# Kernel tuning notes

Measured on AMD Instinct MI355X. Metric: run time of the kernel, lower is better.

Reference implementation:

```python
import jax, jax.numpy as jnp
import numpy as np

B, N, L, E = 4, 8, 2048, 16384
CH = [128, 256, 256, 256]
EPS = 1e-5
USE_MAX = True


def setup_inputs() -> dict:
    key = jax.random.key(0)
    ks = jax.random.split(key, 10)
    d = {}
    d["x"] = jax.random.normal(ks[0], (B, N, CH[0], L), jnp.float32)
    d["edge_index"] = jax.random.randint(ks[1], (2, E), 0, L, dtype=jnp.int32)
    wspecs = [("W1", CH[0], CH[1]), ("W2", CH[1], CH[2]), ("W3", CH[2], CH[3]),
              ("W1s", CH[0], CH[1]), ("W2s", CH[1], CH[2]), ("W3s", CH[2], CH[3])]
    for i, (nm, ci, co) in enumerate(wspecs):
        std = (2.0 / (ci + co)) ** 0.5  # xavier_normal
        d[nm] = std * jax.random.normal(ks[2 + i], (ci, co), jnp.float32)
        d["b" + nm[1:]] = jnp.zeros((co,), jnp.float32)
    for nm, co in [("1", CH[1]), ("2", CH[2]), ("3", CH[3]),
                   ("1s", CH[1]), ("2s", CH[2]), ("3s", CH[3])]:
        d["g" + nm] = jnp.ones((co,), jnp.float32)
        d["be" + nm] = jnp.zeros((co,), jnp.float32)
    return d


def _gcn_norm(edge_index, num_nodes):
    # PyG gcn_norm with improved=True: A_hat = A + 2I, sym normalization.
    src, dst = edge_index[0], edge_index[1]
    loop = jnp.arange(num_nodes, dtype=src.dtype)
    src = jnp.concatenate([src, loop])
    dst = jnp.concatenate([dst, loop])
    w = jnp.concatenate([jnp.ones((edge_index.shape[1],), jnp.float32),
                         jnp.full((num_nodes,), 2.0, jnp.float32)])
    deg = jnp.zeros((num_nodes,), jnp.float32).at[dst].add(w)
    dis = jnp.where(deg > 0, jax.lax.rsqrt(deg), 0.0)
    return src, dst, dis[src] * w * dis[dst]


def _gcn(h, W, bias, src, dst, norm, num_nodes):
    # h: [G, L, Cin] node features for G independent copies of the shared graph
    hw = h @ W  # [G, L, Cout]
    msgs = hw[:, src, :] * norm[None, :, None]  # gather along nodes
    agg = jnp.zeros((h.shape[0], num_nodes, W.shape[1]), h.dtype).at[:, dst].add(msgs)
    return agg + bias


def _bn(x, g, be):
    # x: [Nb, C, L]; training-mode BatchNorm1d over (Nb, L) per channel
    m = x.mean(axis=(0, 2), keepdims=True)
    v = x.var(axis=(0, 2), keepdims=True)
    return g[None, :, None] * (x - m) * jax.lax.rsqrt(v + EPS) + be[None, :, None]


def _forward(x, edge_index, params):
    b, n, c, l = x.shape
    src, dst, norm = _gcn_norm(edge_index, l)
    xo = None
    for (W, bias, Ws, bs, g, be, gs, bes) in params:
        # per-element branch
        h = x.reshape(b * n, x.shape[2], l).transpose(0, 2, 1)  # [b*n, L, C]
        x1 = _gcn(h, W, bias, src, dst, norm, l).transpose(0, 2, 1)  # [b*n, Cout, L]
        x1 = _bn(x1, g, be)
        # symmetric pooled branch
        xp = jnp.max(x, axis=1) if USE_MAX else jnp.sum(x, axis=1)  # [b, C, L]
        x2 = _gcn(xp.transpose(0, 2, 1), Ws, bs, src, dst, norm, l).transpose(0, 2, 1)
        x2 = _bn(x2, gs, bes)
        co = x2.shape[1]
        x2 = jnp.broadcast_to(x2[:, None], (b, n, co, l)).reshape(b * n, co, l)
        xo = jax.nn.relu(x1 + x2)  # [b*n, Cout, L]
        x = xo.reshape(b, n, co, l)
    return xo  # final output is [b*n, CH[3], L] (not reshaped back)


def reference(x, edge_index, W1, b1, W2, b2, W3, b3, W1s, b1s, W2s, b2s, W3s, b3s,
              g1, be1, g2, be2, g3, be3, g1s, be1s, g2s, be2s, g3s, be3s):
    params = [(W1, b1, W1s, b1s, g1, be1, g1s, be1s),
              (W2, b2, W2s, b2s, g2, be2, g2s, be2s),
              (W3, b3, W3s, b3s, g3, be3, g3s, be3s)]
    return _forward(x, edge_index, params)
```

## Files before the change

kernel.cpp:

```cpp
#include <hip/hip_runtime.h>
#include <math.h>

#define LNODES 2048
#define NEDGE 16384
#define GBIG 32
#define GSM 4
#define NCOUT 256
#define BN_EPS 1e-5f
#define ND 32

typedef unsigned short u16;
typedef __attribute__((ext_vector_type(8))) short bf16x8;
typedef __attribute__((ext_vector_type(4))) float f32x4;

__device__ __forceinline__ unsigned pk2(float a, float b) {
  unsigned ua = __float_as_uint(a); ua += 0x7fffu + ((ua >> 16) & 1u);
  unsigned ub = __float_as_uint(b); ub += 0x7fffu + ((ub >> 16) & 1u);
  return (ua >> 16) | (ub & 0xffff0000u);
}
__device__ __forceinline__ float blo(unsigned u) { return __uint_as_float(u << 16); }
__device__ __forceinline__ float bhi(unsigned u) { return __uint_as_float(u & 0xffff0000u); }

__device__ __forceinline__ void gl16(const u16* g, u16* l) {
  __builtin_amdgcn_global_load_lds(
      (const __attribute__((address_space(1))) void*)g,
      (__attribute__((address_space(3))) void*)l, 16, 0, 0);
}


__global__ __launch_bounds__(256) void count_deg_k(const int* __restrict__ ei,
                                                   float* __restrict__ deg,
                                                   int* __restrict__ cnt) {
  int e = blockIdx.x * 256 + threadIdx.x;
  if (e < NEDGE) {
    int d = ei[NEDGE + e];
    atomicAdd(&deg[d], 1.0f);
    atomicAdd(&cnt[d], 1);
  }
}

__global__ __launch_bounds__(256) void dis_k(const float* __restrict__ deg,
                                             float* __restrict__ dis,
                                             float* __restrict__ selfn) {
  int i = blockIdx.x * 256 + threadIdx.x;
  if (i < LNODES) {
    float di = rsqrtf(deg[i] + 2.0f);
    dis[i] = di;
    selfn[i] = 2.0f * di * di;
  }
}

__global__ __launch_bounds__(256) void scan_k(const int* __restrict__ cnt,
                                              int* __restrict__ rp) {
  __shared__ int part[256];
  int t = threadIdx.x;
  int base = t * 8;
  int loc[8];
  int s = 0;
#pragma unroll
  for (int j = 0; j < 8; ++j) { loc[j] = s; s += cnt[base + j]; }
  part[t] = s;
  __syncthreads();
  for (int off = 1; off < 256; off <<= 1) {
    int v = (t >= off) ? part[t - off] : 0;
    __syncthreads();
    part[t] += v;
    __syncthreads();
  }
  int excl = (t == 0) ? 0 : part[t - 1];
#pragma unroll
  for (int j = 0; j < 8; ++j) rp[base + j] = excl + loc[j];
  if (t == 255) rp[LNODES] = part[255];
}

__global__ __launch_bounds__(256) void fill_k(const int* __restrict__ ei,
                                              const int* __restrict__ rp,
                                              int* __restrict__ fillc,
                                              const float* __restrict__ dis,
                                              int* __restrict__ col,
                                              float* __restrict__ wn) {
  int e = blockIdx.x * 256 + threadIdx.x;
  if (e < NEDGE) {
    int s = ei[e], d = ei[NEDGE + e];
    int pos = rp[d] + atomicAdd(&fillc[d], 1);
    col[pos] = s;
    wn[pos] = dis[s] * dis[d];
  }
}

__global__ __launch_bounds__(256) void trans_k(const float* __restrict__ X,
                                               u16* __restrict__ XT, int Cin) {
  __shared__ float T[64][65];
  const int g = blockIdx.z;
  const int n0 = blockIdx.x * 64;
  const int c0 = blockIdx.y * 64;
  const int tr = threadIdx.x >> 4;
  const int tc = (threadIdx.x & 15) * 4;
#pragma unroll
  for (int p = 0; p < 4; ++p) {
    int ci = c0 + tr + p * 16;
    float4 v = *reinterpret_cast<const float4*>(&X[((size_t)g * Cin + ci) * LNODES + n0 + tc]);
    T[tr + p * 16][tc + 0] = v.x; T[tr + p * 16][tc + 1] = v.y;
    T[tr + p * 16][tc + 2] = v.z; T[tr + p * 16][tc + 3] = v.w;
  }
  __syncthreads();
#pragma unroll
  for (int p = 0; p < 4; ++p) {
    int nd = tr + p * 16;
    uint2 o = {pk2(T[tc + 0][nd], T[tc + 1][nd]), pk2(T[tc + 2][nd], T[tc + 3][nd])};
    *reinterpret_cast<uint2*>(&XT[((size_t)g * LNODES + n0 + nd) * Cin + c0 + tc]) = o;
  }
}

struct WCvt {
  const float* src[6];
  u16* dst[6];
  int ci[6];
};
__global__ __launch_bounds__(256) void cvtw_all_k(WCvt wp) {
  __shared__ float T[64][65];
  const int w = blockIdx.z;
  const int Ci = wp.ci[w];
  const int ci0 = blockIdx.y * 64;
  if (ci0 >= Ci) return;
  const float* W = wp.src[w];
  u16* WT = wp.dst[w];
  const int co0 = blockIdx.x * 64;
  const int tr = threadIdx.x >> 4;
  const int tc = (threadIdx.x & 15) * 4;
#pragma unroll
  for (int p = 0; p < 4; ++p) {
    int ci = ci0 + tr + p * 16;
    float4 v = *reinterpret_cast<const float4*>(&W[(size_t)ci * NCOUT + co0 + tc]);
    T[tr + p * 16][tc + 0] = v.x; T[tr + p * 16][tc + 1] = v.y;
    T[tr + p * 16][tc + 2] = v.z; T[tr + p * 16][tc + 3] = v.w;
  }
  __syncthreads();
#pragma unroll
  for (int p = 0; p < 4; ++p) {
    int co = tr + p * 16;
    uint2 o = {pk2(T[tc + 0][co], T[tc + 1][co]), pk2(T[tc + 2][co], T[tc + 3][co])};
    *reinterpret_cast<uint2*>(&WT[(size_t)(co0 + co) * Ci + ci0 + tc]) = o;
  }
}

__global__ __launch_bounds__(256) void pool_bf_k(const u16* __restrict__ X,
                                                 u16* __restrict__ XP, int per) {
  int i = blockIdx.x * 256 + threadIdx.x;
  size_t f = (size_t)i * 8;
  int b = (int)(f / per);
  size_t rem = f - (size_t)b * per;
  const u16* base = X + (size_t)b * 8 * per + rem;
  uint4 u = *reinterpret_cast<const uint4*>(base);
  float m0 = blo(u.x), m1 = bhi(u.x), m2 = blo(u.y), m3 = bhi(u.y);
  float m4 = blo(u.z), m5 = bhi(u.z), m6 = blo(u.w), m7 = bhi(u.w);
#pragma unroll
  for (int j = 1; j < 8; ++j) {
    uint4 v = *reinterpret_cast<const uint4*>(base + (size_t)j * per);
    m0 = fmaxf(m0, blo(v.x)); m1 = fmaxf(m1, bhi(v.x));
    m2 = fmaxf(m2, blo(v.y)); m3 = fmaxf(m3, bhi(v.y));
    m4 = fmaxf(m4, blo(v.z)); m5 = fmaxf(m5, bhi(v.z));
    m6 = fmaxf(m6, blo(v.w)); m7 = fmaxf(m7, bhi(v.w));
  }
  uint4 o = {pk2(m0, m1), pk2(m2, m3), pk2(m4, m5), pk2(m6, m7)};
  *reinterpret_cast<uint4*>(XP + (size_t)b * per + rem) = o;
}

__device__ __forceinline__ void coef_ld(const float* __restrict__ st,
                                        const float* __restrict__ ga,
                                        const float* __restrict__ be,
                                        const float* __restrict__ gs,
                                        const float* __restrict__ bes,
                                        float* lk1, float* lk2, float* lcc, int t) {
  float sA = 0.f, qA = 0.f, sB = 0.f, qB = 0.f;
#pragma unroll
  for (int x = 0; x < 8; ++x) {
    sA += st[x * NCOUT + t];
    qA += st[2048 + x * NCOUT + t];
    sB += st[4096 + x * NCOUT + t];
    qB += st[6144 + x * NCOUT + t];
  }
  const float c1 = (float)(GBIG * LNODES), c2 = (float)(GSM * LNODES);
  float mA = sA / c1;
  float vA = qA / c1 - mA * mA;
  float kA = ga[t] * rsqrtf(vA + BN_EPS);
  float mB = sB / c2;
  float vB = qB / c2 - mB * mB;
  float kB = gs[t] * rsqrtf(vB + BN_EPS);
  lk1[t] = kA;
  lk2[t] = kB;
  lcc[t] = be[t] - kA * mA + bes[t] - kB * mB;
}

template <int Cin>
__global__ __launch_bounds__(256) void gemm_k(const u16* __restrict__ Xbig,
                                              const u16* __restrict__ xp,
                                              const u16* __restrict__ WbT,
                                              const u16* __restrict__ WsT,
                                              u16* __restrict__ HW1,
                                              u16* __restrict__ hw2) {
  __shared__ u16 smem[17408];
  u16* Ash = smem;
  u16* Bsh = smem + 4096;
  const int z = blockIdx.z;
  const bool sym = z < GSM;
  const int g = sym ? z : z - GSM;
  const u16* Wmat = sym ? WsT : WbT;
  const u16* Xmat = sym ? xp : Xbig;
  u16* out = sym ? hw2 : HW1;
  const int n0 = blockIdx.x * 128;
  const int c0 = blockIdx.y * 128;
  const int t = threadIdx.x;
  const int wv = t >> 6;
  const int lane = t & 63;
  const int q = lane >> 4, l = lane & 15;
  const int wm = wv >> 1, wn = wv & 1;
  f32x4 zero = {0.f, 0.f, 0.f, 0.f};
  f32x4 acc[4][4];
#pragma unroll
  for (int i = 0; i < 4; ++i)
#pragma unroll
    for (int j = 0; j < 4; ++j) acc[i][j] = zero;
  const int r0 = t >> 2;
  const int seg = (t & 3) * 8;
  const u16* Wg = Wmat + (size_t)(c0 + r0) * Cin + seg;
  const u16* Xg = Xmat + ((size_t)g * LNODES + n0 + r0) * Cin + seg;
  const size_t rstep = (size_t)64 * Cin;
  for (int k0 = 0; k0 < Cin; k0 += 32) {
    if (k0) __syncthreads();
    gl16(Wg + k0, &Ash[t * 8]);
    gl16(Wg + rstep + k0, &Ash[2048 + t * 8]);
    gl16(Xg + k0, &Bsh[t * 8]);
    gl16(Xg + rstep + k0, &Bsh[2048 + t * 8]);
    __syncthreads();
    bf16x8 af[4], bx[4];
#pragma unroll
    for (int fi = 0; fi < 4; ++fi)
      af[fi] = *reinterpret_cast<const bf16x8*>(&Ash[(wm * 64 + fi * 16 + l) * 32 + q * 8]);
#pragma unroll
    for (int fj = 0; fj < 4; ++fj)
      bx[fj] = *reinterpret_cast<const bf16x8*>(&Bsh[(wn * 64 + fj * 16 + l) * 32 + q * 8]);
#pragma unroll
    for (int fi = 0; fi < 4; ++fi)
#pragma unroll
      for (int fj = 0; fj < 4; ++fj)
        acc[fi][fj] = __builtin_amdgcn_mfma_f32_16x16x32_bf16(af[fi], bx[fj], acc[fi][fj], 0, 0, 0);
  }
  __syncthreads();
  u16* Csh = smem;
#pragma unroll
  for (int fi = 0; fi < 4; ++fi) {
#pragma unroll
    for (int fj = 0; fj < 4; ++fj) {
      int co_l = wm * 64 + fi * 16 + q * 4;
      int nd_l = wn * 64 + fj * 16 + l;
      uint2 pkd = {pk2(acc[fi][fj][0], acc[fi][fj][1]),
                   pk2(acc[fi][fj][2], acc[fi][fj][3])};
      *reinterpret_cast<uint2*>(&Csh[nd_l * 136 + co_l]) = pkd;
    }
  }
  __syncthreads();
#pragma unroll
  for (int p = 0; p < 8; ++p) {
    int idx = p * 256 + t;
    int nd = idx >> 4;
    int c8 = (idx & 15) * 8;
    uint4 v = *reinterpret_cast<const uint4*>(&Csh[nd * 136 + c8]);
    *reinterpret_cast<uint4*>(&out[((size_t)g * LNODES + n0 + nd) * NCOUT + c0 + c8]) = v;
  }
}

__global__ __launch_bounds__(256) void agg_comb_k(const u16* __restrict__ HW1,
                                                  const u16* __restrict__ hw2,
                                                  const int* __restrict__ col,
                                                  const float* __restrict__ wn,
                                                  const int* __restrict__ rp,
                                                  const float* __restrict__ selfn,
                                                  u16* __restrict__ AGG1,
                                                  u16* __restrict__ agg2,
                                                  float* __restrict__ st) {
  __shared__ float lsum[8][NCOUT], lsq[8][NCOUT];
  const int bid = blockIdx.x;
  const int t = threadIdx.x;
  const int wv = t >> 6;
  float* sumO;
  float* sqO;
  int shard;
  if (bid < 1024) {
    int slot = bid >> 3;
    int chunk = slot & 63;
    int g0 = (bid & 7) + 8 * (slot >> 6);
    const int d0 = chunk * ND;
    const int h = (t >> 5) & 1;
    const int ch = (t & 31) * 8;
    const u16* baseh = HW1 + (size_t)(g0 + 16 * h) * LNODES * NCOUT;
    u16* outh = AGG1 + (size_t)(g0 + 16 * h) * LNODES * NCOUT;
    float s0 = 0.f, s1 = 0.f, s2 = 0.f, s3 = 0.f, s4 = 0.f, s5 = 0.f, s6 = 0.f, s7 = 0.f;
    float q0 = 0.f, q1 = 0.f, q2 = 0.f, q3 = 0.f, q4 = 0.f, q5 = 0.f, q6 = 0.f, q7 = 0.f;
    for (int i = wv; i < ND; i += 4) {
      int d = d0 + i;
      int e0 = rp[d], e1 = rp[d + 1];
      float sw = selfn[d];
      uint4 u = *reinterpret_cast<const uint4*>(&baseh[(size_t)d * NCOUT + ch]);
      float a0 = sw * blo(u.x), a1 = sw * bhi(u.x), a2 = sw * blo(u.y), a3 = sw * bhi(u.y);
      float a4 = sw * blo(u.z), a5 = sw * bhi(u.z), a6 = sw * blo(u.w), a7 = sw * bhi(u.w);
      int e = e0;
      const int e4 = e0 + ((e1 - e0) & ~3);
      for (; e < e4; e += 4) {
        int i0 = col[e + 0], i1 = col[e + 1], i2 = col[e + 2], i3 = col[e + 3];
        float w0 = wn[e + 0], w1 = wn[e + 1], w2 = wn[e + 2], w3 = wn[e + 3];
        uint4 v0 = *reinterpret_cast<const uint4*>(&baseh[(size_t)i0 * NCOUT + ch]);
        uint4 v1 = *reinterpret_cast<const uint4*>(&baseh[(size_t)i1 * NCOUT + ch]);
        uint4 v2 = *reinterpret_cast<const uint4*>(&baseh[(size_t)i2 * NCOUT + ch]);
        uint4 v3 = *reinterpret_cast<const uint4*>(&baseh[(size_t)i3 * NCOUT + ch]);
        a0 += w0 * blo(v0.x); a1 += w0 * bhi(v0.x); a2 += w0 * blo(v0.y); a3 += w0 * bhi(v0.y);
        a4 += w0 * blo(v0.z); a5 += w0 * bhi(v0.z); a6 += w0 * blo(v0.w); a7 += w0 * bhi(v0.w);
        a0 += w1 * blo(v1.x); a1 += w1 * bhi(v1.x); a2 += w1 * blo(v1.y); a3 += w1 * bhi(v1.y);
        a4 += w1 * blo(v1.z); a5 += w1 * bhi(v1.z); a6 += w1 * blo(v1.w); a7 += w1 * bhi(v1.w);
        a0 += w2 * blo(v2.x); a1 += w2 * bhi(v2.x); a2 += w2 * blo(v2.y); a3 += w2 * bhi(v2.y);
        a4 += w2 * blo(v2.z); a5 += w2 * bhi(v2.z); a6 += w2 * blo(v2.w); a7 += w2 * bhi(v2.w);
        a0 += w3 * blo(v3.x); a1 += w3 * bhi(v3.x); a2 += w3 * blo(v3.y); a3 += w3 * bhi(v3.y);
        a4 += w3 * blo(v3.z); a5 += w3 * bhi(v3.z); a6 += w3 * blo(v3.w); a7 += w3 * bhi(v3.w);
      }
      for (; e < e1; ++e) {
        int ci = col[e];
        float w = wn[e];
        uint4 v = *reinterpret_cast<const uint4*>(&baseh[(size_t)ci * NCOUT + ch]);
        a0 += w * blo(v.x); a1 += w * bhi(v.x); a2 += w * blo(v.y); a3 += w * bhi(v.y);
        a4 += w * blo(v.z); a5 += w * bhi(v.z); a6 += w * blo(v.w); a7 += w * bhi(v.w);
      }
      uint4 o = {pk2(a0, a1), pk2(a2, a3), pk2(a4, a5), pk2(a6, a7)};
      *reinterpret_cast<uint4*>(&outh[(size_t)d * NCOUT + ch]) = o;
      s0 += a0; s1 += a1; s2 += a2; s3 += a3; s4 += a4; s5 += a5; s6 += a6; s7 += a7;
      q0 += a0 * a0; q1 += a1 * a1; q2 += a2 * a2; q3 += a3 * a3;
      q4 += a4 * a4; q5 += a5 * a5; q6 += a6 * a6; q7 += a7 * a7;
    }
    int row = wv * 2 + h;
    float4 sa = {s0, s1, s2, s3}, sb = {s4, s5, s6, s7};
    float4 qa = {q0, q1, q2, q3}, qb = {q4, q5, q6, q7};
    *reinterpret_cast<float4*>(&lsum[row][ch]) = sa;
    *reinterpret_cast<float4*>(&lsum[row][ch + 4]) = sb;
    *reinterpret_cast<float4*>(&lsq[row][ch]) = qa;
    *reinterpret_cast<float4*>(&lsq[row][ch + 4]) = qb;
    sumO = st; sqO = st + 2048; shard = (bid & 7) * NCOUT;
  } else {
    int b2 = bid - 1024;
    int g = b2 & (GSM - 1);
    int chunk = b2 >> 2;
    const int d0 = chunk * ND;
    const int lc = (t & 63) * 4;
    const u16* base = hw2 + (size_t)g * LNODES * NCOUT;
    float4 s = {0.f, 0.f, 0.f, 0.f}, qq = {0.f, 0.f, 0.f, 0.f};
    for (int i = wv; i < ND; i += 4) {
      int d = d0 + i;
      int e0 = rp[d], e1 = rp[d + 1];
      float sw = selfn[d];
      uint2 u = *reinterpret_cast<const uint2*>(&base[(size_t)d * NCOUT + lc]);
      float4 a = {sw * blo(u.x), sw * bhi(u.x), sw * blo(u.y), sw * bhi(u.y)};
      int e = e0;
      const int e4 = e0 + ((e1 - e0) & ~3);
      for (; e < e4; e += 4) {
        int i0 = col[e + 0], i1 = col[e + 1], i2 = col[e + 2], i3 = col[e + 3];
        float w0 = wn[e + 0], w1 = wn[e + 1], w2 = wn[e + 2], w3 = wn[e + 3];
        uint2 v0 = *reinterpret_cast<const uint2*>(&base[(size_t)i0 * NCOUT + lc]);
        uint2 v1 = *reinterpret_cast<const uint2*>(&base[(size_t)i1 * NCOUT + lc]);
        uint2 v2 = *reinterpret_cast<const uint2*>(&base[(size_t)i2 * NCOUT + lc]);
        uint2 v3 = *reinterpret_cast<const uint2*>(&base[(size_t)i3 * NCOUT + lc]);
        a.x += w0 * blo(v0.x); a.y += w0 * bhi(v0.x); a.z += w0 * blo(v0.y); a.w += w0 * bhi(v0.y);
        a.x += w1 * blo(v1.x); a.y += w1 * bhi(v1.x); a.z += w1 * blo(v1.y); a.w += w1 * bhi(v1.y);
        a.x += w2 * blo(v2.x); a.y += w2 * bhi(v2.x); a.z += w2 * blo(v2.y); a.w += w2 * bhi(v2.y);
        a.x += w3 * blo(v3.x); a.y += w3 * bhi(v3.x); a.z += w3 * blo(v3.y); a.w += w3 * bhi(v3.y);
      }
      for (; e < e1; ++e) {
        float w = wn[e];
        uint2 v = *reinterpret_cast<const uint2*>(&base[(size_t)col[e] * NCOUT + lc]);
        a.x += w * blo(v.x); a.y += w * bhi(v.x); a.z += w * blo(v.y); a.w += w * bhi(v.y);
      }
      uint2 o = {pk2(a.x, a.y), pk2(a.z, a.w)};
      *reinterpret_cast<uint2*>(&agg2[((size_t)g * LNODES + d) * NCOUT + lc]) = o;
      s.x += a.x; s.y += a.y; s.z += a.z; s.w += a.w;
      qq.x += a.x * a.x; qq.y += a.y * a.y; qq.z += a.z * a.z; qq.w += a.w * a.w;
    }
    *reinterpret_cast<float4*>(&lsum[wv][lc]) = s;
    *reinterpret_cast<float4*>(&lsq[wv][lc]) = qq;
    float4 z4 = {0.f, 0.f, 0.f, 0.f};
    *reinterpret_cast<float4*>(&lsum[wv + 4][lc]) = z4;
    *reinterpret_cast<float4*>(&lsq[wv + 4][lc]) = z4;
    sumO = st + 4096; sqO = st + 6144; shard = (b2 & 7) * NCOUT;
  }
  __syncthreads();
  float ts = 0.f, tq = 0.f;
#pragma unroll
  for (int r = 0; r < 8; ++r) {
    ts += lsum[r][t];
    tq += lsq[r][t];
  }
  atomicAdd(&sumO[shard + t], ts);
  atomicAdd(&sqO[shard + t], tq);
}

__global__ __launch_bounds__(256) void fuse_k(const u16* __restrict__ A1,
                                              const u16* __restrict__ A2,
                                              const float* __restrict__ st,
                                              const float* __restrict__ ga,
                                              const float* __restrict__ be,
                                              const float* __restrict__ gs,
                                              const float* __restrict__ bes,
                                              u16* __restrict__ Xf,
                                              u16* __restrict__ xpo) {
  __shared__ __align__(16) float lk1[NCOUT];
  __shared__ __align__(16) float lk2[NCOUT];
  __shared__ __align__(16) float lcc[NCOUT];
  const int t = threadIdx.x;
  coef_ld(st, ga, be, gs, bes, lk1, lk2, lcc, t);
  __syncthreads();
  const int b = blockIdx.y;
  const int idx = blockIdx.x * 256 + t;
  const int node = idx >> 5;
  const int ch = (idx & 31) * 8;
  float K1[8], K2[8], CC[8];
#pragma unroll
  for (int j = 0; j < 8; ++j) {
    K1[j] = lk1[ch + j]; K2[j] = lk2[ch + j]; CC[j] = lcc[ch + j];
  }
  const size_t off2 = ((size_t)b * LNODES + node) * NCOUT + ch;
  uint4 a2 = *reinterpret_cast<const uint4*>(&A2[off2]);
  float t0 = K2[0] * blo(a2.x) + CC[0], t1 = K2[1] * bhi(a2.x) + CC[1];
  float t2 = K2[2] * blo(a2.y) + CC[2], t3 = K2[3] * bhi(a2.y) + CC[3];
  float t4 = K2[4] * blo(a2.z) + CC[4], t5 = K2[5] * bhi(a2.z) + CC[5];
  float t6 = K2[6] * blo(a2.w) + CC[6], t7 = K2[7] * bhi(a2.w) + CC[7];
  float m0 = 0.f, m1 = 0.f, m2 = 0.f, m3 = 0.f, m4 = 0.f, m5 = 0.f, m6 = 0.f, m7 = 0.f;
  const size_t step = (size_t)LNODES * NCOUT;
  const size_t base1 = ((size_t)(b * 8) * LNODES + node) * NCOUT + ch;
#pragma unroll
  for (int n = 0; n < 8; ++n) {
    uint4 a1 = *reinterpret_cast<const uint4*>(&A1[base1 + n * step]);
    float o0 = fmaxf(K1[0] * blo(a1.x) + t0, 0.f);
    float o1 = fmaxf(K1[1] * bhi(a1.x) + t1, 0.f);
    float o2 = fmaxf(K1[2] * blo(a1.y) + t2, 0.f);
    float o3 = fmaxf(K1[3] * bhi(a1.y) + t3, 0.f);
    float o4 = fmaxf(K1[4] * blo(a1.z) + t4, 0.f);
    float o5 = fmaxf(K1[5] * bhi(a1.z) + t5, 0.f);
    float o6 = fmaxf(K1[6] * blo(a1.w) + t6, 0.f);
    float o7 = fmaxf(K1[7] * bhi(a1.w) + t7, 0.f);
    uint4 ov = {pk2(o0, o1), pk2(o2, o3), pk2(o4, o5), pk2(o6, o7)};
    *reinterpret_cast<uint4*>(&Xf[base1 + n * step]) = ov;
    m0 = fmaxf(m0, o0); m1 = fmaxf(m1, o1); m2 = fmaxf(m2, o2); m3 = fmaxf(m3, o3);
    m4 = fmaxf(m4, o4); m5 = fmaxf(m5, o5); m6 = fmaxf(m6, o6); m7 = fmaxf(m7, o7);
  }
  uint4 mo = {pk2(m0, m1), pk2(m2, m3), pk2(m4, m5), pk2(m6, m7)};
  *reinterpret_cast<uint4*>(&xpo[off2]) = mo;
}

__global__ __launch_bounds__(256) void fuse_tr_bf_k(const u16* __restrict__ A1,
                                                    const u16* __restrict__ A2,
                                                    const float* __restrict__ st,
                                                    const float* __restrict__ ga,
                                                    const float* __restrict__ be,
                                                    const float* __restrict__ gs,
                                                    const float* __restrict__ bes,
                                                    float* __restrict__ O) {
  __shared__ float T[64][65];
  __shared__ float lk1[NCOUT], lk2[NCOUT], lcc[NCOUT];
  const int g = blockIdx.z;
  const int d0 = blockIdx.x * 64;
  const int c0 = blockIdx.y * 64;
  const int b = g >> 3;
  const int t = threadIdx.x;
  coef_ld(st, ga, be, gs, bes, lk1, lk2, lcc, t);
  __syncthreads();
  const int tr = t >> 4;
  const int tc = (t & 15) * 4;
#pragma unroll
  for (int p = 0; p < 4; ++p) {
    int d = d0 + tr + p * 16;
    uint2 a1 = *reinterpret_cast<const uint2*>(&A1[((size_t)g * LNODES + d) * NCOUT + c0 + tc]);
    uint2 a2 = *reinterpret_cast<const uint2*>(&A2[((size_t)b * LNODES + d) * NCOUT + c0 + tc]);
    int cb = c0 + tc;
    T[tr + p * 16][tc + 0] = fmaxf(lk1[cb+0] * blo(a1.x) + lk2[cb+0] * blo(a2.x) + lcc[cb+0], 0.f);
    T[tr + p * 16][tc + 1] = fmaxf(lk1[cb+1] * bhi(a1.x) + lk2[cb+1] * bhi(a2.x) + lcc[cb+1], 0.f);
    T[tr + p * 16][tc + 2] = fmaxf(lk1[cb+2] * blo(a1.y) + lk2[cb+2] * blo(a2.y) + lcc[cb+2], 0.f);
    T[tr + p * 16][tc + 3] = fmaxf(lk1[cb+3] * bhi(a1.y) + lk2[cb+3] * bhi(a2.y) + lcc[cb+3], 0.f);
  }
  __syncthreads();
#pragma unroll
  for (int p = 0; p < 4; ++p) {
    int c = tr + p * 16;
    float4 o = {T[tc + 0][c], T[tc + 1][c], T[tc + 2][c], T[tc + 3][c]};
    *reinterpret_cast<float4*>(&O[((size_t)g * NCOUT + c0 + c) * LNODES + d0 + tc]) = o;
  }
}


extern "C" void kernel_launch(void* const* d_in, const int* in_sizes, int n_in,
                              void* d_out, int out_size, void* d_ws, size_t ws_size,
                              hipStream_t stream) {
  const float* x_in = (const float*)d_in[0];
  const int* ei = (const int*)d_in[1];
  const float* W[3]   = {(const float*)d_in[2],  (const float*)d_in[4],  (const float*)d_in[6]};
  const float* Wsym[3]= {(const float*)d_in[8],  (const float*)d_in[10], (const float*)d_in[12]};
  const float* ga[3]  = {(const float*)d_in[14], (const float*)d_in[16], (const float*)d_in[18]};
  const float* be[3]  = {(const float*)d_in[15], (const float*)d_in[17], (const float*)d_in[19]};
  const float* gs[3]  = {(const float*)d_in[20], (const float*)d_in[22], (const float*)d_in[24]};
  const float* bes[3] = {(const float*)d_in[21], (const float*)d_in[23], (const float*)d_in[25]};

  const size_t EBIG = (size_t)GBIG * LNODES * NCOUT;
  const size_t ESM = (size_t)GSM * LNODES * NCOUT;
  char* p = (char*)d_ws;
  u16* XT0  = (u16*)p; p += (size_t)GBIG * LNODES * 128 * 2;
  u16* AGG1 = (u16*)p; p += EBIG * 2;
  u16* agg2 = (u16*)p; p += ESM * 2;
  u16* xp   = (u16*)p; p += ESM * 2;
  u16* hw2  = (u16*)p; p += ESM * 2;
  u16* WbT[3], *WsT[3];
  for (int i = 0; i < 3; ++i) { WbT[i] = (u16*)p; p += NCOUT * NCOUT * 2; }
  for (int i = 0; i < 3; ++i) { WsT[i] = (u16*)p; p += NCOUT * NCOUT * 2; }
  int*   rp   = (int*)p;   p += 2064 * 4;
  float* dis  = (float*)p; p += LNODES * 4;
  float* selfn= (float*)p; p += LNODES * 4;
  char* zbase = p;
  float* deg  = (float*)p; p += LNODES * 4;
  int*   cnt  = (int*)p;   p += LNODES * 4;
  int*   fillc= (int*)p;   p += LNODES * 4;
  int*   col  = (int*)p;   p += (NEDGE + 8) * 4;
  float* wn   = (float*)p; p += (NEDGE + 8) * 4;
  float* stats= (float*)p; p += 3 * 4 * 2048 * 4;
  size_t zsize = (size_t)(p - zbase);

  u16* HW1 = (u16*)d_out;
  u16* Xf  = (u16*)d_out + EBIG;
  float* stL[3] = {stats, stats + 8192, stats + 16384};

  hipMemsetAsync(zbase, 0, zsize, stream);
  count_deg_k<<<NEDGE / 256, 256, 0, stream>>>(ei, deg, cnt);
  dis_k<<<LNODES / 256, 256, 0, stream>>>(deg, dis, selfn);
  scan_k<<<1, 256, 0, stream>>>(cnt, rp);
  fill_k<<<NEDGE / 256, 256, 0, stream>>>(ei, rp, fillc, dis, col, wn);
  WCvt wc;
  for (int i = 0; i < 3; ++i) {
    wc.src[i] = W[i];     wc.dst[i] = WbT[i];     wc.ci[i] = (i == 0) ? 128 : 256;
    wc.src[3 + i] = Wsym[i]; wc.dst[3 + i] = WsT[i]; wc.ci[3 + i] = (i == 0) ? 128 : 256;
  }
  cvtw_all_k<<<dim3(4, 4, 6), 256, 0, stream>>>(wc);
  trans_k<<<dim3(LNODES / 64, 128 / 64, GBIG), 256, 0, stream>>>(x_in, XT0, 128);
  pool_bf_k<<<GSM * 128 * LNODES / 8 / 256, 256, 0, stream>>>(XT0, xp, 128 * LNODES);

  dim3 ggrid(LNODES / 128, NCOUT / 128, GBIG + GSM);
  dim3 fgrid(LNODES * NCOUT / 8 / 256, GSM);
  gemm_k<128><<<ggrid, 256, 0, stream>>>(XT0, xp, WbT[0], WsT[0], HW1, hw2);
  agg_comb_k<<<1280, 256, 0, stream>>>(HW1, hw2, col, wn, rp, selfn, AGG1, agg2, stL[0]);
  fuse_k<<<fgrid, 256, 0, stream>>>(AGG1, agg2, stL[0], ga[0], be[0], gs[0], bes[0], Xf, xp);
  gemm_k<256><<<ggrid, 256, 0, stream>>>(Xf, xp, WbT[1], WsT[1], HW1, hw2);
  agg_comb_k<<<1280, 256, 0, stream>>>(HW1, hw2, col, wn, rp, selfn, AGG1, agg2, stL[1]);
  fuse_k<<<fgrid, 256, 0, stream>>>(AGG1, agg2, stL[1], ga[1], be[1], gs[1], bes[1], Xf, xp);
  gemm_k<256><<<ggrid, 256, 0, stream>>>(Xf, xp, WbT[2], WsT[2], HW1, hw2);
  agg_comb_k<<<1280, 256, 0, stream>>>(HW1, hw2, col, wn, rp, selfn, AGG1, agg2, stL[2]);
  fuse_tr_bf_k<<<dim3(LNODES / 64, NCOUT / 64, GBIG), 256, 0, stream>>>(
      AGG1, agg2, stL[2], ga[2], be[2], gs[2], bes[2], (float*)d_out);
}
```

Baseline: 347.6 us.

## Fuse BN+ReLU+max-pool prologue into GEMM, keep full-K activation tile in LDS

Drops the separate fuse_k pass. The GEMM now applies the batch-norm affine, residual add, ReLU and (for the pooled branch) max over the N elements while loading its activation tile, then stores the whole 128xCin tile into XOR-swizzled LDS. This removes the write and re-read of the intermediate Xf and pooled buffers, and the weight fragments are now read straight from global memory instead of through staged LDS tiles. In exchange, each column block (blockIdx.y) recomputes the prologue, and the pooled-branch blocks read all 8 per-element tiles. LDS use grows to 64KB, which may lower occupancy.

```diff
diff --git a/kernel.cpp b/kernel.cpp
--- a/kernel.cpp
+++ b/kernel.cpp
@@ -20,12 +20,6 @@
 }
 __device__ __forceinline__ float blo(unsigned u) { return __uint_as_float(u << 16); }
 __device__ __forceinline__ float bhi(unsigned u) { return __uint_as_float(u & 0xffff0000u); }
-
-__device__ __forceinline__ void gl16(const u16* g, u16* l) {
-  __builtin_amdgcn_global_load_lds(
-      (const __attribute__((address_space(1))) void*)g,
-      (__attribute__((address_space(3))) void*)l, 16, 0, 0);
-}
 
 
 __global__ __launch_bounds__(256) void count_deg_k(const int* __restrict__ ei,
@@ -192,25 +186,99 @@
   lcc[t] = be[t] - kA * mA + bes[t] - kB * mB;
 }
 
-template <int Cin>
-__global__ __launch_bounds__(256) void gemm_k(const u16* __restrict__ Xbig,
-                                              const u16* __restrict__ xp,
-                                              const u16* __restrict__ WbT,
-                                              const u16* __restrict__ WsT,
-                                              u16* __restrict__ HW1,
-                                              u16* __restrict__ hw2) {
-  __shared__ u16 smem[17408];
-  u16* Ash = smem;
-  u16* Bsh = smem + 4096;
+template <int MODE>
+__global__ __launch_bounds__(256) void gemm2_k(const u16* __restrict__ B1,
+                                               const u16* __restrict__ B2,
+                                               const float* __restrict__ st,
+                                               const float* __restrict__ ga,
+                                               const float* __restrict__ be,
+                                               const float* __restrict__ gs,
+                                               const float* __restrict__ bes,
+                                               const u16* __restrict__ WbT,
+                                               const u16* __restrict__ WsT,
+                                               u16* __restrict__ HW1,
+                                               u16* __restrict__ hw2) {
+  constexpr int Cin = (MODE == 0) ? 128 : 256;
+  constexpr int SMSZ = (128 * Cin > 17408) ? 128 * Cin : 17408;
+  __shared__ u16 smem[SMSZ];
+  __shared__ float lk1[NCOUT], lk2[NCOUT], lcc[NCOUT];
   const int z = blockIdx.z;
   const bool sym = z < GSM;
   const int g = sym ? z : z - GSM;
   const u16* Wmat = sym ? WsT : WbT;
-  const u16* Xmat = sym ? xp : Xbig;
   u16* out = sym ? hw2 : HW1;
   const int n0 = blockIdx.x * 128;
   const int c0 = blockIdx.y * 128;
   const int t = threadIdx.x;
+  constexpr int OPR = Cin / 8;
+  constexpr int RPI = 256 / OPR;
+  constexpr int NIT = 128 / RPI;
+  const int ro = t / OPR;
+  const int ch8 = (t % OPR) * 8;
+
+  float K1[8], K2[8], CC[8];
+  if constexpr (MODE == 1) {
+    coef_ld(st, ga, be, gs, bes, lk1, lk2, lcc, t);
+    __syncthreads();
+#pragma unroll
+    for (int j = 0; j < 8; ++j) { K1[j] = lk1[ch8 + j]; K2[j] = lk2[ch8 + j]; CC[j] = lcc[ch8 + j]; }
+  }
+
+#define BIDX(r, c) ((((r) * Cin) + (c)) ^ (((r) & 7) << 3))
+
+  if constexpr (MODE == 0) {
+    const u16* src = (sym ? B2 : B1) + (size_t)g * LNODES * Cin;
+#pragma unroll
+    for (int it = 0; it < NIT; ++it) {
+      int row = it * RPI + ro;
+      uint4 v = *reinterpret_cast<const uint4*>(&src[(size_t)(n0 + row) * Cin + ch8]);
+      *reinterpret_cast<uint4*>(&smem[BIDX(row, ch8)]) = v;
+    }
+  } else if (!sym) {
+    const size_t b1o = ((size_t)g * LNODES + n0) * NCOUT + ch8;
+    const size_t b2o = ((size_t)(g >> 3) * LNODES + n0) * NCOUT + ch8;
+#pragma unroll
+    for (int it = 0; it < NIT; ++it) {
+      int row = it * RPI + ro;
+      uint4 a1 = *reinterpret_cast<const uint4*>(&B1[b1o + (size_t)row * NCOUT]);
+      uint4 a2 = *reinterpret_cast<const uint4*>(&B2[b2o + (size_t)row * NCOUT]);
+      float o0 = fmaxf(K1[0] * blo(a1.x) + K2[0] * blo(a2.x) + CC[0], 0.f);
+      float o1 = fmaxf(K1[1] * bhi(a1.x) + K2[1] * bhi(a2.x) + CC[1], 0.f);
+      float o2 = fmaxf(K1[2] * blo(a1.y) + K2[2] * blo(a2.y) + CC[2], 0.f);
+      float o3 = fmaxf(K1[3] * bhi(a1.y) + K2[3] * bhi(a2.y) + CC[3], 0.f);
+      float o4 = fmaxf(K1[4] * blo(a1.z) + K2[4] * blo(a2.z) + CC[4], 0.f);
+      float o5 = fmaxf(K1[5] * bhi(a1.z) + K2[5] * bhi(a2.z) + CC[5], 0.f);
+      float o6 = fmaxf(K1[6] * blo(a1.w) + K2[6] * blo(a2.w) + CC[6], 0.f);
+      float o7 = fmaxf(K1[7] * bhi(a1.w) + K2[7] * bhi(a2.w) + CC[7], 0.f);
+      uint4 ov = {pk2(o0, o1), pk2(o2, o3), pk2(o4, o5), pk2(o6, o7)};
+      *reinterpret_cast<uint4*>(&smem[BIDX(row, ch8)]) = ov;
+    }
+  } else {
+    const size_t b2o = ((size_t)g * LNODES + n0) * NCOUT + ch8;
+    const size_t a1b = ((size_t)(g * 8) * LNODES + n0) * NCOUT + ch8;
+    const size_t nstep = (size_t)LNODES * NCOUT;
+    for (int it = 0; it < NIT; ++it) {
+      int row = it * RPI + ro;
+      uint4 a2 = *reinterpret_cast<const uint4*>(&B2[b2o + (size_t)row * NCOUT]);
+      float t0 = K2[0] * blo(a2.x) + CC[0], t1 = K2[1] * bhi(a2.x) + CC[1];
+      float t2 = K2[2] * blo(a2.y) + CC[2], t3 = K2[3] * bhi(a2.y) + CC[3];
+      float t4 = K2[4] * blo(a2.z) + CC[4], t5 = K2[5] * bhi(a2.z) + CC[5];
+      float t6 = K2[6] * blo(a2.w) + CC[6], t7 = K2[7] * bhi(a2.w) + CC[7];
+      float m0 = 0.f, m1 = 0.f, m2 = 0.f, m3 = 0.f, m4 = 0.f, m5 = 0.f, m6 = 0.f, m7 = 0.f;
+#pragma unroll
+      for (int n = 0; n < 8; ++n) {
+        uint4 a1 = *reinterpret_cast<const uint4*>(&B1[a1b + n * nstep + (size_t)row * NCOUT]);
+        m0 = fmaxf(m0, K1[0] * blo(a1.x) + t0); m1 = fmaxf(m1, K1[1] * bhi(a1.x) + t1);
+        m2 = fmaxf(m2, K1[2] * blo(a1.y) + t2); m3 = fmaxf(m3, K1[3] * bhi(a1.y) + t3);
+        m4 = fmaxf(m4, K1[4] * blo(a1.z) + t4); m5 = fmaxf(m5, K1[5] * bhi(a1.z) + t5);
+        m6 = fmaxf(m6, K1[6] * blo(a1.w) + t6); m7 = fmaxf(m7, K1[7] * bhi(a1.w) + t7);
+      }
+      uint4 ov = {pk2(m0, m1), pk2(m2, m3), pk2(m4, m5), pk2(m6, m7)};
+      *reinterpret_cast<uint4*>(&smem[BIDX(row, ch8)]) = ov;
+    }
+  }
+  __syncthreads();
+
   const int wv = t >> 6;
   const int lane = t & 63;
   const int q = lane >> 4, l = lane & 15;
@@ -221,31 +289,27 @@
   for (int i = 0; i < 4; ++i)
 #pragma unroll
     for (int j = 0; j < 4; ++j) acc[i][j] = zero;
-  const int r0 = t >> 2;
-  const int seg = (t & 3) * 8;
-  const u16* Wg = Wmat + (size_t)(c0 + r0) * Cin + seg;
-  const u16* Xg = Xmat + ((size_t)g * LNODES + n0 + r0) * Cin + seg;
-  const size_t rstep = (size_t)64 * Cin;
+
+  const u16* Wfrag = Wmat + (size_t)(c0 + wm * 64 + l) * Cin + q * 8;
+#pragma unroll
   for (int k0 = 0; k0 < Cin; k0 += 32) {
-    if (k0) __syncthreads();
-    gl16(Wg + k0, &Ash[t * 8]);
-    gl16(Wg + rstep + k0, &Ash[2048 + t * 8]);
-    gl16(Xg + k0, &Bsh[t * 8]);
-    gl16(Xg + rstep + k0, &Bsh[2048 + t * 8]);
-    __syncthreads();
     bf16x8 af[4], bx[4];
 #pragma unroll
     for (int fi = 0; fi < 4; ++fi)
-      af[fi] = *reinterpret_cast<const bf16x8*>(&Ash[(wm * 64 + fi * 16 + l) * 32 + q * 8]);
-#pragma unroll
-    for (int fj = 0; fj < 4; ++fj)
-      bx[fj] = *reinterpret_cast<const bf16x8*>(&Bsh[(wn * 64 + fj * 16 + l) * 32 + q * 8]);
+      af[fi] = *reinterpret_cast<const bf16x8*>(&Wfrag[(size_t)(fi * 16) * Cin + k0]);
+#pragma unroll
+    for (int fj = 0; fj < 4; ++fj) {
+      int brow = wn * 64 + fj * 16 + l;
+      bx[fj] = *reinterpret_cast<const bf16x8*>(&smem[(brow * Cin + k0 + q * 8) ^ ((brow & 7) << 3)]);
+    }
 #pragma unroll
     for (int fi = 0; fi < 4; ++fi)
 #pragma unroll
       for (int fj = 0; fj < 4; ++fj)
         acc[fi][fj] = __builtin_amdgcn_mfma_f32_16x16x32_bf16(af[fi], bx[fj], acc[fi][fj], 0, 0, 0);
   }
+#undef BIDX
+
   __syncthreads();
   u16* Csh = smem;
 #pragma unroll
@@ -399,59 +463,6 @@
   atomicAdd(&sqO[shard + t], tq);
 }
 
-__global__ __launch_bounds__(256) void fuse_k(const u16* __restrict__ A1,
-                                              const u16* __restrict__ A2,
-                                              const float* __restrict__ st,
-                                              const float* __restrict__ ga,
-                                              const float* __restrict__ be,
-                                              const float* __restrict__ gs,
-                                              const float* __restrict__ bes,
-                                              u16* __restrict__ Xf,
-                                              u16* __restrict__ xpo) {
-  __shared__ __align__(16) float lk1[NCOUT];
-  __shared__ __align__(16) float lk2[NCOUT];
-  __shared__ __align__(16) float lcc[NCOUT];
-  const int t = threadIdx.x;
-  coef_ld(st, ga, be, gs, bes, lk1, lk2, lcc, t);
-  __syncthreads();
-  const int b = blockIdx.y;
-  const int idx = blockIdx.x * 256 + t;
-  const int node = idx >> 5;
-  const int ch = (idx & 31) * 8;
-  float K1[8], K2[8], CC[8];
-#pragma unroll
-  for (int j = 0; j < 8; ++j) {
-    K1[j] = lk1[ch + j]; K2[j] = lk2[ch + j]; CC[j] = lcc[ch + j];
-  }
-  const size_t off2 = ((size_t)b * LNODES + node) * NCOUT + ch;
-  uint4 a2 = *reinterpret_cast<const uint4*>(&A2[off2]);
-  float t0 = K2[0] * blo(a2.x) + CC[0], t1 = K2[1] * bhi(a2.x) + CC[1];
-  float t2 = K2[2] * blo(a2.y) + CC[2], t3 = K2[3] * bhi(a2.y) + CC[3];
-  float t4 = K2[4] * blo(a2.z) + CC[4], t5 = K2[5] * bhi(a2.z) + CC[5];
-  float t6 = K2[6] * blo(a2.w) + CC[6], t7 = K2[7] * bhi(a2.w) + CC[7];
-  float m0 = 0.f, m1 = 0.f, m2 = 0.f, m3 = 0.f, m4 = 0.f, m5 = 0.f, m6 = 0.f, m7 = 0.f;
-  const size_t step = (size_t)LNODES * NCOUT;
-  const size_t base1 = ((size_t)(b * 8) * LNODES + node) * NCOUT + ch;
-#pragma unroll
-  for (int n = 0; n < 8; ++n) {
-    uint4 a1 = *reinterpret_cast<const uint4*>(&A1[base1 + n * step]);
-    float o0 = fmaxf(K1[0] * blo(a1.x) + t0, 0.f);
-    float o1 = fmaxf(K1[1] * bhi(a1.x) + t1, 0.f);
-    float o2 = fmaxf(K1[2] * blo(a1.y) + t2, 0.f);
-    float o3 = fmaxf(K1[3] * bhi(a1.y) + t3, 0.f);
-    float o4 = fmaxf(K1[4] * blo(a1.z) + t4, 0.f);
-    float o5 = fmaxf(K1[5] * bhi(a1.z) + t5, 0.f);
-    float o6 = fmaxf(K1[6] * blo(a1.w) + t6, 0.f);
-    float o7 = fmaxf(K1[7] * bhi(a1.w) + t7, 0.f);
-    uint4 ov = {pk2(o0, o1), pk2(o2, o3), pk2(o4, o5), pk2(o6, o7)};
-    *reinterpret_cast<uint4*>(&Xf[base1 + n * step]) = ov;
-    m0 = fmaxf(m0, o0); m1 = fmaxf(m1, o1); m2 = fmaxf(m2, o2); m3 = fmaxf(m3, o3);
-    m4 = fmaxf(m4, o4); m5 = fmaxf(m5, o5); m6 = fmaxf(m6, o6); m7 = fmaxf(m7, o7);
-  }
-  uint4 mo = {pk2(m0, m1), pk2(m2, m3), pk2(m4, m5), pk2(m6, m7)};
-  *reinterpret_cast<uint4*>(&xpo[off2]) = mo;
-}
-
 __global__ __launch_bounds__(256) void fuse_tr_bf_k(const u16* __restrict__ A1,
                                                     const u16* __restrict__ A2,
                                                     const float* __restrict__ st,
@@ -528,7 +539,6 @@
   size_t zsize = (size_t)(p - zbase);
 
   u16* HW1 = (u16*)d_out;
-  u16* Xf  = (u16*)d_out + EBIG;
   float* stL[3] = {stats, stats + 8192, stats + 16384};
 
   hipMemsetAsync(zbase, 0, zsize, stream);
@@ -546,14 +556,14 @@
   pool_bf_k<<<GSM * 128 * LNODES / 8 / 256, 256, 0, stream>>>(XT0, xp, 128 * LNODES);
 
   dim3 ggrid(LNODES / 128, NCOUT / 128, GBIG + GSM);
-  dim3 fgrid(LNODES * NCOUT / 8 / 256, GSM);
-  gemm_k<128><<<ggrid, 256, 0, stream>>>(XT0, xp, WbT[0], WsT[0], HW1, hw2);
+  gemm2_k<0><<<ggrid, 256, 0, stream>>>(XT0, xp, nullptr, nullptr, nullptr, nullptr,
+                                        nullptr, WbT[0], WsT[0], HW1, hw2);
   agg_comb_k<<<1280, 256, 0, stream>>>(HW1, hw2, col, wn, rp, selfn, AGG1, agg2, stL[0]);
-  fuse_k<<<fgrid, 256, 0, stream>>>(AGG1, agg2, stL[0], ga[0], be[0], gs[0], bes[0], Xf, xp);
-  gemm_k<256><<<ggrid, 256, 0, stream>>>(Xf, xp, WbT[1], WsT[1], HW1, hw2);
+  gemm2_k<1><<<ggrid, 256, 0, stream>>>(AGG1, agg2, stL[0], ga[0], be[0], gs[0], bes[0],
+                                        WbT[1], WsT[1], HW1, hw2);
   agg_comb_k<<<1280, 256, 0, stream>>>(HW1, hw2, col, wn, rp, selfn, AGG1, agg2, stL[1]);
-  fuse_k<<<fgrid, 256, 0, stream>>>(AGG1, agg2, stL[1], ga[1], be[1], gs[1], bes[1], Xf, xp);
-  gemm_k<256><<<ggrid, 256, 0, stream>>>(Xf, xp, WbT[2], WsT[2], HW1, hw2);
+  gemm2_k<1><<<ggrid, 256, 0, stream>>>(AGG1, agg2, stL[1], ga[1], be[1], gs[1], bes[1],
+                                        WbT[2], WsT[2], HW1, hw2);
   agg_comb_k<<<1280, 256, 0, stream>>>(HW1, hw2, col, wn, rp, selfn, AGG1, agg2, stL[2]);
   fuse_tr_bf_k<<<dim3(LNODES / 64, NCOUT / 64, GBIG), 256, 0, stream>>>(
       AGG1, agg2, stL[2], ga[2], be[2], gs[2], bes[2], (float*)d_out);
```

After: 365.5 us. 1.05x slower.
